# Kernel optimization log

Measured on AMD Instinct MI355X. Metric: run time of the kernel, lower is better.

## Reference

```python
import jax, jax.numpy as jnp
import numpy as np

B, L, D = 8, 4096, 1024
POOL = 5          # pool_size
EPS = 1e-6
BOUNDARY_P = 1.0 / 16.0


def setup_inputs() -> dict:
    key = jax.random.key(0)
    k1, k2, k3, k4, k5 = jax.random.split(key, 5)
    frame_embeddings = jax.random.normal(k1, (B, L, D), jnp.float32)
    boundary_mask = jax.random.bernoulli(k2, BOUNDARY_P, (B, L))
    change_score = jax.random.uniform(k3, (B, L), jnp.float32)
    boundary_confidence = jax.random.uniform(k4, (B, L), jnp.float32)
    W = jax.random.normal(k5, (D, D), jnp.float32) * 0.02
    b = jnp.zeros((D,), jnp.float32)
    return {
        "frame_embeddings": frame_embeddings,
        "boundary_mask": boundary_mask,
        "change_score": change_score,
        "boundary_confidence": boundary_confidence,
        "W": W,
        "b": b,
    }


def reference(frame_embeddings, boundary_mask, change_score, boundary_confidence, W, b):
    Bb, Ll, Dd = frame_embeddings.shape
    window = POOL

    # --- windowed weighted pooling at EVERY position via cumsum differences ---
    w = change_score                                    # use_change_score=True
    weighted = frame_embeddings * w[..., None]          # (B, L, D)
    Cv = jnp.concatenate([jnp.zeros((Bb, 1, Dd), weighted.dtype),
                          jnp.cumsum(weighted, axis=1)], axis=1)   # (B, L+1, D)
    Cw = jnp.concatenate([jnp.zeros((Bb, 1), w.dtype),
                          jnp.cumsum(w, axis=1)], axis=1)          # (B, L+1)
    t = jnp.arange(Ll)
    start = jnp.maximum(0, t - window + 1)              # segment = [start, t]
    pooled_all = jnp.take(Cv, t + 1, axis=1) - jnp.take(Cv, start, axis=1)  # (B,L,D)
    wsum = jnp.take(Cw, t + 1, axis=1) - jnp.take(Cw, start, axis=1)        # (B,L)
    pooled_all = pooled_all / (wsum[..., None] + EPS)   # normalize=True

    # --- pack boundary positions into contiguous slots (ragged -> padded) ---
    counts = jnp.sum(boundary_mask, axis=1)                      # (B,)
    max_units = max(int(np.asarray(counts).max()), 1)
    dest = jnp.where(boundary_mask, jnp.cumsum(boundary_mask, axis=1) - 1, max_units)

    def pack(vals, d):  # vals: (L, ...) -> (max_units+1, ...); last row is dump slot
        return jnp.zeros((max_units + 1,) + vals.shape[1:], vals.dtype).at[d].set(vals)

    packed = jax.vmap(pack)(pooled_all, dest)[:, :max_units]           # (B,U,D)
    idx = jax.vmap(pack)(jnp.broadcast_to(t, (Bb, Ll)), dest)[:, :max_units]
    conf = jax.vmap(pack)(boundary_confidence, dest)[:, :max_units]
    slot_mask = jnp.arange(max_units)[None, :] < counts[:, None]       # (B,U)

    # --- linear projection applied only to real pooled vectors ---
    chunks = packed @ W.T + b
    chunks = jnp.where(slot_mask[..., None], chunks, 0.0)
    return chunks, slot_mask, idx, conf
```

## Files before the change

### kernel.cpp

```cpp
#include <hip/hip_runtime.h>


#define B_ 8
#define L_ 4096
#define D_ 1024
#define POOLW 5
#define EPS_ 1e-6f
#define KSPLIT 4
#define KCHUNK (D_ / KSPLIT)
#define NB_ 16

typedef __attribute__((ext_vector_type(8))) short bf16x8;
typedef __attribute__((ext_vector_type(4))) float f32x4;

__device__ __forceinline__ unsigned short bf16_rne(float v) {
    unsigned u = __float_as_uint(v);
    unsigned r = u + 0x7FFFu + ((u >> 16) & 1u);
    return (unsigned short)(r >> 16);
}
__device__ __forceinline__ float bf16_f32(unsigned short h) {
    return __uint_as_float(((unsigned)h) << 16);
}

__device__ __forceinline__ size_t packed_off(int m, int k) {
    return (size_t)(m >> 4) * (16 * D_) + (size_t)(k >> 5) * 512 +
           (size_t)(((m & 15) + 16 * ((k >> 3) & 3)) * 8 + (k & 7));
}

__device__ __forceinline__ int mask_val(const void* mask, int flag, int i) {
    if (flag == 0) return ((const unsigned char*)mask)[i] != 0;
    if (flag == 1) return ((const int*)mask)[i] != 0;
    return ((const float*)mask)[i] != 0.0f;
}

__global__ __launch_bounds__(256) void pack_kernel(
    const void* __restrict__ mask, const float* __restrict__ conf_in,
    int* __restrict__ counts, int* __restrict__ t_idx,
    float* __restrict__ out_mask, float* __restrict__ out_idx,
    float* __restrict__ out_conf, int U) {
    const int b   = blockIdx.x;
    const int tid = threadIdx.x;
    __shared__ int s_clo, s_chi, s_flag;
    __shared__ int scan[256];
    if (tid == 0) { s_clo = 0; s_chi = 0; }
    __syncthreads();
    const uint4 wv = ((const uint4*)mask)[b * 256 + tid];
    const unsigned wd[4] = {wv.x, wv.y, wv.z, wv.w};
    int clo = 0, chi = 0;
#pragma unroll
    for (int i = 0; i < 4; ++i) {
        clo += ((wd[i] & 0x000000FFu) != 0u);
        chi += ((wd[i] & 0xFFFFFF00u) != 0u);
    }
    if (clo) atomicAdd(&s_clo, clo);
    if (chi) atomicAdd(&s_chi, chi);
    for (int u = tid; u < U; u += 256) {
        out_mask[b * U + u] = 0.0f;
        out_idx[b * U + u]  = 0.0f;
        out_conf[b * U + u] = 0.0f;
    }
    __syncthreads();
    if (tid == 0) s_flag = (s_chi == 0) ? 1 : ((s_clo == 0) ? 2 : 0);
    __syncthreads();
    const int flag = s_flag;
    const int base = b * L_;
    int vals[16];
    int cnt = 0;
#pragma unroll
    for (int j = 0; j < 16; ++j) {
        int v = mask_val(mask, flag, base + tid * 16 + j);
        vals[j] = v;
        cnt += v;
    }
    scan[tid] = cnt;
    __syncthreads();
    for (int off = 1; off < 256; off <<= 1) {
        int v   = scan[tid];
        int add = (tid >= off) ? scan[tid - off] : 0;
        __syncthreads();
        scan[tid] = v + add;
        __syncthreads();
    }
    const int excl = scan[tid] - cnt;
    if (tid == 0) counts[b] = scan[255];
    int u = excl;
#pragma unroll
    for (int j = 0; j < 16; ++j) {
        if (vals[j]) {
            const int t = tid * 16 + j;
            t_idx[b * U + u]    = t;
            out_mask[b * U + u] = 1.0f;
            out_idx[b * U + u]  = (float)t;
            out_conf[b * U + u] = conf_in[base + t];
            ++u;
        }
    }
}

__global__ __launch_bounds__(256) void wconv_kernel(
    const float* __restrict__ W, unsigned short* __restrict__ Whi,
    unsigned short* __restrict__ Wlo) {
    const int i = (blockIdx.x * 256 + threadIdx.x) * 4;
    const int n = i >> 10, k = i & 1023;
    const float4 v = *(const float4*)&W[i];
    ushort4 hi, lo;
    hi.x = bf16_rne(v.x); lo.x = bf16_rne(v.x - bf16_f32(hi.x));
    hi.y = bf16_rne(v.y); lo.y = bf16_rne(v.y - bf16_f32(hi.y));
    hi.z = bf16_rne(v.z); lo.z = bf16_rne(v.z - bf16_f32(hi.z));
    hi.w = bf16_rne(v.w); lo.w = bf16_rne(v.w - bf16_f32(hi.w));
    const size_t o = packed_off(n, k);
    *(ushort4*)&Whi[o] = hi;
    *(ushort4*)&Wlo[o] = lo;
}

__global__ __launch_bounds__(256) void pool_kernel(
    const float* __restrict__ emb, const float* __restrict__ cs,
    const int* __restrict__ counts, const int* __restrict__ t_idx,
    unsigned short* __restrict__ Phi, unsigned short* __restrict__ Plo,
    int U) {
    const int m = blockIdx.x;
    const int b = m / U, u = m - b * U;
    if (u >= counts[b]) return;
    const int t     = t_idx[m];
    const int start = (t - POOLW + 1) > 0 ? (t - POOLW + 1) : 0;
    float wsum = 0.f;
    for (int s = start; s <= t; ++s) wsum += cs[b * L_ + s];
    const float inv = 1.0f / (wsum + EPS_);
    const int d0 = threadIdx.x * 4;
    float4 acc = make_float4(0.f, 0.f, 0.f, 0.f);
    for (int s = start; s <= t; ++s) {
        const float w  = cs[b * L_ + s];
        const float4 e = *(const float4*)&emb[((size_t)(b * L_ + s)) * D_ + d0];
        acc.x += w * e.x; acc.y += w * e.y; acc.z += w * e.z; acc.w += w * e.w;
    }
    acc.x *= inv; acc.y *= inv; acc.z *= inv; acc.w *= inv;
    ushort4 hi, lo;
    hi.x = bf16_rne(acc.x); lo.x = bf16_rne(acc.x - bf16_f32(hi.x));
    hi.y = bf16_rne(acc.y); lo.y = bf16_rne(acc.y - bf16_f32(hi.y));
    hi.z = bf16_rne(acc.z); lo.z = bf16_rne(acc.z - bf16_f32(hi.z));
    hi.w = bf16_rne(acc.w); lo.w = bf16_rne(acc.w - bf16_f32(hi.w));
    const size_t o = packed_off(m, d0);
    *(ushort4*)&Phi[o] = hi;
    *(ushort4*)&Plo[o] = lo;
}

__global__ __launch_bounds__(256) void gemm_kernel(
    const unsigned short* __restrict__ Phi, const unsigned short* __restrict__ Plo,
    const unsigned short* __restrict__ Whi, const unsigned short* __restrict__ Wlo,
    const float* __restrict__ bias, const int* __restrict__ counts,
    float* __restrict__ C, int M, int U, int MB) {
    const int nwg = MB * KSPLIT * NB_;
    const int q = nwg >> 3, r = nwg & 7;
    const int xcd = blockIdx.x & 7, pos = blockIdx.x >> 3;
    const int wg =
        (xcd < r ? xcd * (q + 1) : r * (q + 1) + (xcd - r) * q) + pos;
    const int mt  = wg / (KSPLIT * NB_);
    const int rem = wg - mt * (KSPLIT * NB_);
    const int kt  = rem >> 4;
    const int nt  = rem & 15;

    const int tid  = threadIdx.x;
    const int w    = tid >> 6;
    const int lane = tid & 63;
    const int bm = mt * 64, bn = nt * 64, k0 = kt * KCHUNK;
    const int wm = (w >> 1) * 32, wn = (w & 1) * 32;

    const int amt = (bm + wm) >> 4;
    const int bnt = (bn + wn) >> 4;
    size_t aoff0 = (size_t)amt * (16 * D_) + (size_t)(k0 >> 5) * 512 + lane * 8;
    size_t aoff1 = aoff0 + (size_t)(16 * D_);
    size_t boff0 = (size_t)bnt * (16 * D_) + (size_t)(k0 >> 5) * 512 + lane * 8;
    size_t boff1 = boff0 + (size_t)(16 * D_);

    f32x4 acc[2][2] = {};
#pragma unroll
    for (int ks = 0; ks < KCHUNK / 32; ++ks) {
        const size_t sa = (size_t)ks * 512;
        bf16x8 ah0 = *(const bf16x8*)(Phi + aoff0 + sa);
        bf16x8 ah1 = *(const bf16x8*)(Phi + aoff1 + sa);
        bf16x8 al0 = *(const bf16x8*)(Plo + aoff0 + sa);
        bf16x8 al1 = *(const bf16x8*)(Plo + aoff1 + sa);
        bf16x8 bh0 = *(const bf16x8*)(Whi + boff0 + sa);
        bf16x8 bh1 = *(const bf16x8*)(Whi + boff1 + sa);
        bf16x8 bl0 = *(const bf16x8*)(Wlo + boff0 + sa);
        bf16x8 bl1 = *(const bf16x8*)(Wlo + boff1 + sa);
        __builtin_amdgcn_s_setprio(1);
        acc[0][0] = __builtin_amdgcn_mfma_f32_16x16x32_bf16(ah0, bh0, acc[0][0], 0, 0, 0);
        acc[0][1] = __builtin_amdgcn_mfma_f32_16x16x32_bf16(ah0, bh1, acc[0][1], 0, 0, 0);
        acc[1][0] = __builtin_amdgcn_mfma_f32_16x16x32_bf16(ah1, bh0, acc[1][0], 0, 0, 0);
        acc[1][1] = __builtin_amdgcn_mfma_f32_16x16x32_bf16(ah1, bh1, acc[1][1], 0, 0, 0);
        acc[0][0] = __builtin_amdgcn_mfma_f32_16x16x32_bf16(ah0, bl0, acc[0][0], 0, 0, 0);
        acc[0][1] = __builtin_amdgcn_mfma_f32_16x16x32_bf16(ah0, bl1, acc[0][1], 0, 0, 0);
        acc[1][0] = __builtin_amdgcn_mfma_f32_16x16x32_bf16(ah1, bl0, acc[1][0], 0, 0, 0);
        acc[1][1] = __builtin_amdgcn_mfma_f32_16x16x32_bf16(ah1, bl1, acc[1][1], 0, 0, 0);
        acc[0][0] = __builtin_amdgcn_mfma_f32_16x16x32_bf16(al0, bh0, acc[0][0], 0, 0, 0);
        acc[0][1] = __builtin_amdgcn_mfma_f32_16x16x32_bf16(al0, bh1, acc[0][1], 0, 0, 0);
        acc[1][0] = __builtin_amdgcn_mfma_f32_16x16x32_bf16(al1, bh0, acc[1][0], 0, 0, 0);
        acc[1][1] = __builtin_amdgcn_mfma_f32_16x16x32_bf16(al1, bh1, acc[1][1], 0, 0, 0);
        __builtin_amdgcn_s_setprio(0);
    }
    const int lr = lane & 15;
#pragma unroll
    for (int i = 0; i < 2; ++i)
#pragma unroll
        for (int j = 0; j < 2; ++j) {
            const int n  = bn + wn + j * 16 + lr;
            const float bv = (kt == 0) ? bias[n] : 0.0f;
#pragma unroll
            for (int rr = 0; rr < 4; ++rr) {
                const int m = bm + wm + i * 16 + (lane >> 4) * 4 + rr;
                if (m >= M) continue;
                const int b_ = m / U;
                const int u  = m - b_ * U;
                if (u < counts[b_])
                    atomicAdd(&C[(size_t)m * D_ + n], acc[i][j][rr] + bv);
            }
        }
}

extern "C" void kernel_launch(void* const* d_in, const int* in_sizes, int n_in,
                              void* d_out, int out_size, void* d_ws,
                              size_t ws_size, hipStream_t stream) {
    const float* emb     = (const float*)d_in[0];
    const void*  mask    = d_in[1];
    const float* cs      = (const float*)d_in[2];
    const float* conf_in = (const float*)d_in[3];
    const float* W       = (const float*)d_in[4];
    const float* bias    = (const float*)d_in[5];

    const int U    = out_size / (B_ * (D_ + 3));
    const int M    = B_ * U;
    const int Mpad = (M + 63) & ~63;

    float* out_chunks = (float*)d_out;
    float* out_mask   = out_chunks + (size_t)M * D_;
    float* out_idx    = out_mask + M;
    float* out_conf   = out_idx + M;

    char* ws = (char*)d_ws;
    int* counts = (int*)ws;
    int* t_idx  = (int*)(ws + 256);
    size_t off  = (256 + (size_t)Mpad * 4 + 255) & ~(size_t)255;
    unsigned short* Phi = (unsigned short*)(ws + off);
    off += (size_t)Mpad * D_ * 2;
    unsigned short* Plo = (unsigned short*)(ws + off);
    off += (size_t)Mpad * D_ * 2;
    unsigned short* Whi = (unsigned short*)(ws + off);
    off += (size_t)D_ * D_ * 2;
    unsigned short* Wlo = (unsigned short*)(ws + off);

    hipMemsetAsync(out_chunks, 0, (size_t)M * D_ * sizeof(float), stream);

    pack_kernel<<<B_, 256, 0, stream>>>(mask, conf_in, counts, t_idx,
                                        out_mask, out_idx, out_conf, U);
    wconv_kernel<<<D_ * D_ / 1024, 256, 0, stream>>>(W, Whi, Wlo);
    pool_kernel<<<M, 256, 0, stream>>>(emb, cs, counts, t_idx, Phi, Plo, U);
    const int MB = Mpad / 64;
    gemm_kernel<<<MB * KSPLIT * NB_, 256, 0, stream>>>(
        Phi, Plo, Whi, Wlo, bias, counts, out_chunks, M, U, MB);
}
```

Before: 256.0 us.

## Enlarge GEMM tile to 128x128 with 64x64 warp tiles and register double-buffering

Each wave now computes a 64x64 output block (4x4 MFMA fragments) instead of 32x32, so each workgroup covers a 128x128 tile and loaded fragments are reused across more MFMAs. Fragment loads for the next k-step are issued ahead of the current MFMAs through two register sets, to hide global-load latency. The cost is much higher register pressure (two fragment sets plus 64 accumulator floats per lane), which may lower occupancy. The grid also shrinks, and since M is only about 8*U, padding to 128 rows may waste more work.

New measurement: 312.1 us. 21.9% more time.

```diff
diff --git a/kernel.cpp b/kernel.cpp
--- a/kernel.cpp
+++ b/kernel.cpp
@@ -8,7 +8,7 @@
 #define EPS_ 1e-6f
 #define KSPLIT 4
 #define KCHUNK (D_ / KSPLIT)
-#define NB_ 16
+#define NB_ 8
 
 typedef __attribute__((ext_vector_type(8))) short bf16x8;
 typedef __attribute__((ext_vector_type(4))) float f32x4;
@@ -144,6 +144,44 @@
     *(ushort4*)&Plo[o] = lo;
 }
 
+struct Frag {
+    bf16x8 ah[4], al[4], bh[4], bl[4];
+};
+
+__device__ __forceinline__ void load_set(
+    Frag& f, const unsigned short* __restrict__ Phi,
+    const unsigned short* __restrict__ Plo,
+    const unsigned short* __restrict__ Whi,
+    const unsigned short* __restrict__ Wlo, size_t abase, size_t bbase,
+    int ks) {
+    const size_t s = (size_t)ks * 512;
+#pragma unroll
+    for (int i = 0; i < 4; ++i) {
+        const size_t ao = abase + (size_t)i * (16 * D_) + s;
+        const size_t bo = bbase + (size_t)i * (16 * D_) + s;
+        f.ah[i] = *(const bf16x8*)(Phi + ao);
+        f.al[i] = *(const bf16x8*)(Plo + ao);
+        f.bh[i] = *(const bf16x8*)(Whi + bo);
+        f.bl[i] = *(const bf16x8*)(Wlo + bo);
+    }
+}
+
+__device__ __forceinline__ void mfma_set(const Frag& f, f32x4 acc[4][4]) {
+    __builtin_amdgcn_s_setprio(1);
+#pragma unroll
+    for (int i = 0; i < 4; ++i)
+#pragma unroll
+        for (int j = 0; j < 4; ++j) {
+            acc[i][j] = __builtin_amdgcn_mfma_f32_16x16x32_bf16(
+                f.ah[i], f.bh[j], acc[i][j], 0, 0, 0);
+            acc[i][j] = __builtin_amdgcn_mfma_f32_16x16x32_bf16(
+                f.ah[i], f.bl[j], acc[i][j], 0, 0, 0);
+            acc[i][j] = __builtin_amdgcn_mfma_f32_16x16x32_bf16(
+                f.al[i], f.bh[j], acc[i][j], 0, 0, 0);
+        }
+    __builtin_amdgcn_s_setprio(0);
+}
+
 __global__ __launch_bounds__(256) void gemm_kernel(
     const unsigned short* __restrict__ Phi, const unsigned short* __restrict__ Plo,
     const unsigned short* __restrict__ Whi, const unsigned short* __restrict__ Wlo,
@@ -156,59 +194,42 @@
         (xcd < r ? xcd * (q + 1) : r * (q + 1) + (xcd - r) * q) + pos;
     const int mt  = wg / (KSPLIT * NB_);
     const int rem = wg - mt * (KSPLIT * NB_);
-    const int kt  = rem >> 4;
-    const int nt  = rem & 15;
+    const int kt  = rem >> 3;
+    const int nt  = rem & 7;
 
     const int tid  = threadIdx.x;
     const int w    = tid >> 6;
     const int lane = tid & 63;
-    const int bm = mt * 64, bn = nt * 64, k0 = kt * KCHUNK;
-    const int wm = (w >> 1) * 32, wn = (w & 1) * 32;
-
-    const int amt = (bm + wm) >> 4;
-    const int bnt = (bn + wn) >> 4;
-    size_t aoff0 = (size_t)amt * (16 * D_) + (size_t)(k0 >> 5) * 512 + lane * 8;
-    size_t aoff1 = aoff0 + (size_t)(16 * D_);
-    size_t boff0 = (size_t)bnt * (16 * D_) + (size_t)(k0 >> 5) * 512 + lane * 8;
-    size_t boff1 = boff0 + (size_t)(16 * D_);
-
-    f32x4 acc[2][2] = {};
-#pragma unroll
-    for (int ks = 0; ks < KCHUNK / 32; ++ks) {
-        const size_t sa = (size_t)ks * 512;
-        bf16x8 ah0 = *(const bf16x8*)(Phi + aoff0 + sa);
-        bf16x8 ah1 = *(const bf16x8*)(Phi + aoff1 + sa);
-        bf16x8 al0 = *(const bf16x8*)(Plo + aoff0 + sa);
-        bf16x8 al1 = *(const bf16x8*)(Plo + aoff1 + sa);
-        bf16x8 bh0 = *(const bf16x8*)(Whi + boff0 + sa);
-        bf16x8 bh1 = *(const bf16x8*)(Whi + boff1 + sa);
-        bf16x8 bl0 = *(const bf16x8*)(Wlo + boff0 + sa);
-        bf16x8 bl1 = *(const bf16x8*)(Wlo + boff1 + sa);
-        __builtin_amdgcn_s_setprio(1);
-        acc[0][0] = __builtin_amdgcn_mfma_f32_16x16x32_bf16(ah0, bh0, acc[0][0], 0, 0, 0);
-        acc[0][1] = __builtin_amdgcn_mfma_f32_16x16x32_bf16(ah0, bh1, acc[0][1], 0, 0, 0);
-        acc[1][0] = __builtin_amdgcn_mfma_f32_16x16x32_bf16(ah1, bh0, acc[1][0], 0, 0, 0);
-        acc[1][1] = __builtin_amdgcn_mfma_f32_16x16x32_bf16(ah1, bh1, acc[1][1], 0, 0, 0);
-        acc[0][0] = __builtin_amdgcn_mfma_f32_16x16x32_bf16(ah0, bl0, acc[0][0], 0, 0, 0);
-        acc[0][1] = __builtin_amdgcn_mfma_f32_16x16x32_bf16(ah0, bl1, acc[0][1], 0, 0, 0);
-        acc[1][0] = __builtin_amdgcn_mfma_f32_16x16x32_bf16(ah1, bl0, acc[1][0], 0, 0, 0);
-        acc[1][1] = __builtin_amdgcn_mfma_f32_16x16x32_bf16(ah1, bl1, acc[1][1], 0, 0, 0);
-        acc[0][0] = __builtin_amdgcn_mfma_f32_16x16x32_bf16(al0, bh0, acc[0][0], 0, 0, 0);
-        acc[0][1] = __builtin_amdgcn_mfma_f32_16x16x32_bf16(al0, bh1, acc[0][1], 0, 0, 0);
-        acc[1][0] = __builtin_amdgcn_mfma_f32_16x16x32_bf16(al1, bh0, acc[1][0], 0, 0, 0);
-        acc[1][1] = __builtin_amdgcn_mfma_f32_16x16x32_bf16(al1, bh1, acc[1][1], 0, 0, 0);
-        __builtin_amdgcn_s_setprio(0);
+    const int bm = mt * 128, bn = nt * 128, k0 = kt * KCHUNK;
+    const int wm = (w >> 1) * 64, wn = (w & 1) * 64;
+
+    const size_t abase =
+        (size_t)((bm + wm) >> 4) * (16 * D_) + (size_t)(k0 >> 5) * 512 + lane * 8;
+    const size_t bbase =
+        (size_t)((bn + wn) >> 4) * (16 * D_) + (size_t)(k0 >> 5) * 512 + lane * 8;
+
+    f32x4 acc[4][4] = {};
+    Frag f0, f1;
+    load_set(f0, Phi, Plo, Whi, Wlo, abase, bbase, 0);
+#pragma unroll
+    for (int ks = 0; ks < KCHUNK / 32; ks += 2) {
+        load_set(f1, Phi, Plo, Whi, Wlo, abase, bbase, ks + 1);
+        mfma_set(f0, acc);
+        if (ks + 2 < KCHUNK / 32)
+            load_set(f0, Phi, Plo, Whi, Wlo, abase, bbase, ks + 2);
+        mfma_set(f1, acc);
     }
     const int lr = lane & 15;
-#pragma unroll
-    for (int i = 0; i < 2; ++i)
-#pragma unroll
-        for (int j = 0; j < 2; ++j) {
+    const int mrow = (lane >> 4) * 4;
+#pragma unroll
+    for (int i = 0; i < 4; ++i)
+#pragma unroll
+        for (int j = 0; j < 4; ++j) {
             const int n  = bn + wn + j * 16 + lr;
             const float bv = (kt == 0) ? bias[n] : 0.0f;
 #pragma unroll
             for (int rr = 0; rr < 4; ++rr) {
-                const int m = bm + wm + i * 16 + (lane >> 4) * 4 + rr;
+                const int m = bm + wm + i * 16 + mrow + rr;
                 if (m >= M) continue;
                 const int b_ = m / U;
                 const int u  = m - b_ * U;
@@ -230,7 +251,7 @@
 
     const int U    = out_size / (B_ * (D_ + 3));
     const int M    = B_ * U;
-    const int Mpad = (M + 63) & ~63;
+    const int Mpad = (M + 127) & ~127;
 
     float* out_chunks = (float*)d_out;
     float* out_mask   = out_chunks + (size_t)M * D_;
@@ -255,7 +276,7 @@
                                         out_mask, out_idx, out_conf, U);
     wconv_kernel<<<D_ * D_ / 1024, 256, 0, stream>>>(W, Whi, Wlo);
     pool_kernel<<<M, 256, 0, stream>>>(emb, cs, counts, t_idx, Phi, Plo, U);
-    const int MB = Mpad / 64;
+    const int MB = Mpad / 128;
     gemm_kernel<<<MB * KSPLIT * NB_, 256, 0, stream>>>(
         Phi, Plo, Whi, Wlo, bias, counts, out_chunks, M, U, MB);
 }
```
